# Optimization experiments

Measured on AMD Instinct MI355X. Metric: run time of the kernel, lower is better.

## Reference

```python
import jax, jax.numpy as jnp
import numpy as np

KSIZE = 7
LOSS_WEIGHT = 1.0


def _box_filter(x, ksize):
    # x: (N, 1, H, W) already reflect-padded -> valid conv with ones kernel
    kern = jnp.ones((1, 1, ksize, ksize), x.dtype)
    return jax.lax.conv_general_dilated(
        x, kern, window_strides=(1, 1), padding='VALID',
        dimension_numbers=('NCHW', 'OIHW', 'NCHW'))


def _local_var(residual, ksize):
    # unbiased variance over each ksize x ksize window (reflect padding),
    # computed via box-filtered sum and sum-of-squares (same math as
    # torch.var over unfolded windows, without materializing the windows).
    pad = (ksize - 1) // 2
    rp = jnp.pad(residual, ((0, 0), (0, 0), (pad, pad), (pad, pad)), mode='reflect')
    n = ksize * ksize
    s = _box_filter(rp, ksize)        # window sums
    ss = _box_filter(rp * rp, ksize)  # window sums of squares
    return (ss - s * s / n) / (n - 1)


def setup_inputs() -> dict:
    key = jax.random.key(0)
    k1, k2 = jax.random.split(key)
    shape = (16, 3, 512, 512)
    pred = jax.random.normal(k1, shape, dtype=jnp.float32)
    target = jax.random.normal(k2, shape, dtype=jnp.float32)
    return {"pred": pred, "target": target}


def reference(pred, target):
    # residual over channels: (N, 1, H, W)
    residual = jnp.sum(jnp.abs(target - pred), axis=1, keepdims=True)
    # patch-level weight: unbiased var over (C,H,W), ^(1/5)
    patch_w = jnp.var(residual, axis=(1, 2, 3), keepdims=True, ddof=1) ** 0.2
    # pixel-level weight: local unbiased variance in ksize window
    pixel_w = _local_var(residual, KSIZE)
    overall_weight = patch_w * pixel_w  # (N, 1, H, W), broadcasts over C
    # L1 criterion on weighted pred vs weighted target
    return jnp.mean(jnp.abs(overall_weight * pred - overall_weight * target)) * LOSS_WEIGHT
```

## Files before the change

### kernel.cpp

```cpp
#include <hip/hip_runtime.h>
#include <math.h>

#define N_IMG 16
#define C_CH 3
#define H_DIM 512
#define W_DIM 512
#define HW (H_DIM * W_DIM)
#define KS 7
#define PAD 3

#define TS 32
#define TILE (TS + 2 * PAD)
#define TSTRIDE 40
#define TPB 256
#define TILES_PER_IMG ((H_DIM / TS) * (W_DIM / TS))
#define NBLOCKS (N_IMG * TILES_PER_IMG)


__global__ __launch_bounds__(TPB) void k_fused(const float* __restrict__ pred,
                                               const float* __restrict__ targ,
                                               float* __restrict__ pr,
                                               float* __restrict__ pr2,
                                               float* __restrict__ pc) {
    __shared__ float tile[TILE * TSTRIDE];

    const int bid = blockIdx.x;
    const int n   = bid >> 8;
    const int t   = bid & 255;
    const int by  = t >> 4;
    const int bx  = t & 15;
    const int tid = threadIdx.x;

    const float* p = pred + (size_t)n * C_CH * HW;
    const float* q = targ + (size_t)n * C_CH * HW;

    for (int i = tid; i < TILE * TILE; i += TPB) {
        const int ly = i / TILE;
        const int lx = i - ly * TILE;
        int gy = by * TS - PAD + ly;
        int gx = bx * TS - PAD + lx;
        gy = (gy < 0) ? -gy : ((gy >= H_DIM) ? (2 * H_DIM - 2 - gy) : gy);
        gx = (gx < 0) ? -gx : ((gx >= W_DIM) ? (2 * W_DIM - 2 - gx) : gx);
        const int off = gy * W_DIM + gx;
        const float r = fabsf(q[off] - p[off])
                      + fabsf(q[off + HW] - p[off + HW])
                      + fabsf(q[off + 2 * HW] - p[off + 2 * HW]);
        tile[ly * TSTRIDE + lx] = r;
    }
    __syncthreads();

    const int tx  = tid & 31;
    const int ty0 = (tid >> 5) << 2;

    float colS[KS], colSS[KS];
#pragma unroll
    for (int j = 0; j < KS; ++j) {
        float s = 0.f, ss = 0.f;
#pragma unroll
        for (int dy = 0; dy < KS; ++dy) {
            const float v = tile[(ty0 + dy) * TSTRIDE + tx + j];
            s  += v;
            ss += v * v;
        }
        colS[j] = s; colSS[j] = ss;
    }

    float acc_r = 0.f, acc_r2 = 0.f, acc_c = 0.f;

#pragma unroll
    for (int k = 0; k < 4; ++k) {
        if (k > 0) {
#pragma unroll
            for (int j = 0; j < KS; ++j) {
                const float vn = tile[(ty0 + 6 + k) * TSTRIDE + tx + j];
                const float vo = tile[(ty0 + k - 1) * TSTRIDE + tx + j];
                colS[j]  += vn - vo;
                colSS[j] += vn * vn - vo * vo;
            }
        }
        float S = 0.f, SS = 0.f;
#pragma unroll
        for (int j = 0; j < KS; ++j) { S += colS[j]; SS += colSS[j]; }

        const float pix_var = (SS - S * S * (1.0f / 49.0f)) * (1.0f / 48.0f);
        const float center  = tile[(ty0 + 3 + k) * TSTRIDE + tx + 3];

        acc_r  += center;
        acc_r2 += center * center;
        acc_c  += pix_var * center;
    }

#pragma unroll
    for (int off = 32; off > 0; off >>= 1) {
        acc_r  += __shfl_down(acc_r,  off);
        acc_r2 += __shfl_down(acc_r2, off);
        acc_c  += __shfl_down(acc_c,  off);
    }
    __shared__ float sh_r[4], sh_r2[4], sh_c[4];
    const int lane = tid & 63;
    const int wave = tid >> 6;
    if (lane == 0) { sh_r[wave] = acc_r; sh_r2[wave] = acc_r2; sh_c[wave] = acc_c; }
    __syncthreads();
    if (tid == 0) {
        pr [bid] = sh_r [0] + sh_r [1] + sh_r [2] + sh_r [3];
        pr2[bid] = sh_r2[0] + sh_r2[1] + sh_r2[2] + sh_r2[3];
        pc [bid] = sh_c [0] + sh_c [1] + sh_c [2] + sh_c [3];
    }
}

__global__ void k_final(const float* __restrict__ pr,
                        const float* __restrict__ pr2,
                        const float* __restrict__ pc,
                        float* __restrict__ out) {
    __shared__ double sh[N_IMG];
    const int tid  = threadIdx.x;
    const int w    = tid >> 6;
    const int lane = tid & 63;

    double R = 0.0, R2 = 0.0, Cs = 0.0;
    for (int i = lane; i < TILES_PER_IMG; i += 64) {
        const int idx = w * TILES_PER_IMG + i;
        R  += (double)pr[idx];
        R2 += (double)pr2[idx];
        Cs += (double)pc[idx];
    }
#pragma unroll
    for (int off = 32; off > 0; off >>= 1) {
        R  += __shfl_down(R,  off);
        R2 += __shfl_down(R2, off);
        Cs += __shfl_down(Cs, off);
    }
    if (lane == 0) {
        const double pvar = (R2 - R * R / (double)HW) / (double)(HW - 1);
        sh[w] = pow(pvar, 0.2) * Cs;
    }
    __syncthreads();
    if (tid == 0) {
        double s = 0.0;
        for (int i = 0; i < N_IMG; ++i) s += sh[i];
        out[0] = (float)(s / ((double)N_IMG * C_CH * HW));
    }
}

extern "C" void kernel_launch(void* const* d_in, const int* in_sizes, int n_in,
                              void* d_out, int out_size, void* d_ws, size_t ws_size,
                              hipStream_t stream) {
    const float* pred = (const float*)d_in[0];
    const float* targ = (const float*)d_in[1];

    float* pr  = (float*)d_ws;
    float* pr2 = pr  + NBLOCKS;
    float* pc  = pr2 + NBLOCKS;
    float* out = (float*)d_out;

    k_fused<<<NBLOCKS, TPB, 0, stream>>>(pred, targ, pr, pr2, pc);
    k_final<<<1, 1024, 0, stream>>>(pr, pr2, pc, out);
}
```

Baseline: 144.7 us.

## Enlarge tiles to 64x64 and switch to row-sum sliding window

Tile size grows from 32 to 64, so the reflect halo is a smaller fraction of each tile and fewer global loads are redundant. Each thread now walks 16 rows instead of 4 and keeps a ring buffer of per-row horizontal sums, updating the running window sum and sum of squares with one new row per step. The load loop is unrolled with a fixed trip count, and the final reduction is simplified for 64 tiles per image. Fewer blocks (1024) may lower occupancy and latency hiding, and longer running-sum chains slightly change float rounding.

Measured after the change: 126.8 us. 12.4% less time.

```diff
diff --git a/kernel.cpp b/kernel.cpp
--- a/kernel.cpp
+++ b/kernel.cpp
@@ -9,9 +9,9 @@
 #define KS 7
 #define PAD 3
 
-#define TS 32
+#define TS 64
 #define TILE (TS + 2 * PAD)
-#define TSTRIDE 40
+#define TSTRIDE 72
 #define TPB 256
 #define TILES_PER_IMG ((H_DIM / TS) * (W_DIM / TS))
 #define NBLOCKS (N_IMG * TILES_PER_IMG)
@@ -25,63 +25,85 @@
     __shared__ float tile[TILE * TSTRIDE];
 
     const int bid = blockIdx.x;
-    const int n   = bid >> 8;
-    const int t   = bid & 255;
-    const int by  = t >> 4;
-    const int bx  = t & 15;
+    const int n   = bid >> 6;
+    const int t   = bid & 63;
+    const int by  = t >> 3;
+    const int bx  = t & 7;
     const int tid = threadIdx.x;
 
-    const float* p = pred + (size_t)n * C_CH * HW;
-    const float* q = targ + (size_t)n * C_CH * HW;
+    const float* p0 = pred + (size_t)n * C_CH * HW;
+    const float* p1 = p0 + HW;
+    const float* p2 = p1 + HW;
+    const float* q0 = targ + (size_t)n * C_CH * HW;
+    const float* q1 = q0 + HW;
+    const float* q2 = q1 + HW;
 
-    for (int i = tid; i < TILE * TILE; i += TPB) {
+    const int y0 = by * TS - PAD;
+    const int x0 = bx * TS - PAD;
+#pragma unroll 4
+    for (int it = 0; it < 19; ++it) {
+        const int i  = tid + it * TPB;
         const int ly = i / TILE;
         const int lx = i - ly * TILE;
-        int gy = by * TS - PAD + ly;
-        int gx = bx * TS - PAD + lx;
+        int gy = y0 + ly;
+        int gx = x0 + lx;
         gy = (gy < 0) ? -gy : ((gy >= H_DIM) ? (2 * H_DIM - 2 - gy) : gy);
         gx = (gx < 0) ? -gx : ((gx >= W_DIM) ? (2 * W_DIM - 2 - gx) : gx);
         const int off = gy * W_DIM + gx;
-        const float r = fabsf(q[off] - p[off])
-                      + fabsf(q[off + HW] - p[off + HW])
-                      + fabsf(q[off + 2 * HW] - p[off + 2 * HW]);
-        tile[ly * TSTRIDE + lx] = r;
+        tile[ly * TSTRIDE + lx] = fabsf(q0[off] - p0[off])
+                                + fabsf(q1[off] - p1[off])
+                                + fabsf(q2[off] - p2[off]);
+    }
+    if (tid < 36) {
+        const int i  = tid + 19 * TPB;
+        const int ly = i / TILE;
+        const int lx = i - ly * TILE;
+        int gy = y0 + ly;
+        int gx = x0 + lx;
+        gy = (gy < 0) ? -gy : ((gy >= H_DIM) ? (2 * H_DIM - 2 - gy) : gy);
+        gx = (gx < 0) ? -gx : ((gx >= W_DIM) ? (2 * W_DIM - 2 - gx) : gx);
+        const int off = gy * W_DIM + gx;
+        tile[ly * TSTRIDE + lx] = fabsf(q0[off] - p0[off])
+                                + fabsf(q1[off] - p1[off])
+                                + fabsf(q2[off] - p2[off]);
     }
     __syncthreads();
 
-    const int tx  = tid & 31;
-    const int ty0 = (tid >> 5) << 2;
+    const int tx  = tid & 63;
+    const int ty0 = (tid >> 6) << 4;
 
-    float colS[KS], colSS[KS];
+    float rS[KS], rSS[KS];
+    float S = 0.f, SS = 0.f;
 #pragma unroll
-    for (int j = 0; j < KS; ++j) {
+    for (int dy = 0; dy < KS; ++dy) {
         float s = 0.f, ss = 0.f;
 #pragma unroll
-        for (int dy = 0; dy < KS; ++dy) {
+        for (int j = 0; j < KS; ++j) {
             const float v = tile[(ty0 + dy) * TSTRIDE + tx + j];
             s  += v;
             ss += v * v;
         }
-        colS[j] = s; colSS[j] = ss;
+        rS[dy] = s; rSS[dy] = ss;
+        S += s; SS += ss;
     }
 
     float acc_r = 0.f, acc_r2 = 0.f, acc_c = 0.f;
 
 #pragma unroll
-    for (int k = 0; k < 4; ++k) {
+    for (int k = 0; k < 16; ++k) {
         if (k > 0) {
+            float s = 0.f, ss = 0.f;
 #pragma unroll
             for (int j = 0; j < KS; ++j) {
-                const float vn = tile[(ty0 + 6 + k) * TSTRIDE + tx + j];
-                const float vo = tile[(ty0 + k - 1) * TSTRIDE + tx + j];
-                colS[j]  += vn - vo;
-                colSS[j] += vn * vn - vo * vo;
+                const float v = tile[(ty0 + 6 + k) * TSTRIDE + tx + j];
+                s  += v;
+                ss += v * v;
             }
+            const int slot = (k - 1) % KS;
+            S  += s  - rS[slot];
+            SS += ss - rSS[slot];
+            rS[slot] = s; rSS[slot] = ss;
         }
-        float S = 0.f, SS = 0.f;
-#pragma unroll
-        for (int j = 0; j < KS; ++j) { S += colS[j]; SS += colSS[j]; }
-
         const float pix_var = (SS - S * S * (1.0f / 49.0f)) * (1.0f / 48.0f);
         const float center  = tile[(ty0 + 3 + k) * TSTRIDE + tx + 3];
 
@@ -118,11 +140,11 @@
     const int lane = tid & 63;
 
     double R = 0.0, R2 = 0.0, Cs = 0.0;
-    for (int i = lane; i < TILES_PER_IMG; i += 64) {
-        const int idx = w * TILES_PER_IMG + i;
-        R  += (double)pr[idx];
-        R2 += (double)pr2[idx];
-        Cs += (double)pc[idx];
+    if (lane < TILES_PER_IMG) {
+        const int idx = w * TILES_PER_IMG + lane;
+        R  = (double)pr[idx];
+        R2 = (double)pr2[idx];
+        Cs = (double)pc[idx];
     }
 #pragma unroll
     for (int off = 32; off > 0; off >>= 1) {
```

## Use 64x32 tiles with float4 loads and sliding row-sum box filter

Applied to the files above, without the earlier changes.

Widens each tile to 64x32 pixels, so the reflect-padded halo is a smaller share of each tile. The interior residual is loaded with float4 vector reads of pred and target, and the left and right halo columns are filled by scalar loads. The 7x7 window now slides vertically over cached per-row sums instead of per-column sums, and each thread handles 8 output rows instead of 4. The aim is fewer global memory transactions and less redundant shared-memory and ALU work, at the cost of more registers and half as many blocks.

Result: faster. 127.4 us (-11.9%).

```diff
diff --git a/kernel.cpp b/kernel.cpp
--- a/kernel.cpp
+++ b/kernel.cpp
@@ -9,82 +9,100 @@
 #define KS 7
 #define PAD 3
 
-#define TS 32
-#define TILE (TS + 2 * PAD)
-#define TSTRIDE 40
+#define TSX 64
+#define TSY 32
+#define TILE_H (TSY + 2 * PAD)
+#define TSTRIDE 72
 #define TPB 256
-#define TILES_PER_IMG ((H_DIM / TS) * (W_DIM / TS))
+#define TILES_X (W_DIM / TSX)
+#define TILES_Y (H_DIM / TSY)
+#define TILES_PER_IMG (TILES_X * TILES_Y)
 #define NBLOCKS (N_IMG * TILES_PER_IMG)
 
+__device__ __forceinline__ int reflect_i(int g, int n) {
+    return (g < 0) ? -g : ((g >= n) ? (2 * n - 2 - g) : g);
+}
 
 __global__ __launch_bounds__(TPB) void k_fused(const float* __restrict__ pred,
                                                const float* __restrict__ targ,
                                                float* __restrict__ pr,
                                                float* __restrict__ pr2,
                                                float* __restrict__ pc) {
-    __shared__ float tile[TILE * TSTRIDE];
+    __shared__ __align__(16) float tile[TILE_H * TSTRIDE];
 
     const int bid = blockIdx.x;
-    const int n   = bid >> 8;
-    const int t   = bid & 255;
-    const int by  = t >> 4;
-    const int bx  = t & 15;
+    const int n   = bid >> 7;
+    const int t   = bid & 127;
+    const int by  = t >> 3;
+    const int bx  = t & 7;
     const int tid = threadIdx.x;
 
-    const float* p = pred + (size_t)n * C_CH * HW;
-    const float* q = targ + (size_t)n * C_CH * HW;
+    const int y0 = by * TSY - PAD;
 
-    for (int i = tid; i < TILE * TILE; i += TPB) {
-        const int ly = i / TILE;
-        const int lx = i - ly * TILE;
-        int gy = by * TS - PAD + ly;
-        int gx = bx * TS - PAD + lx;
-        gy = (gy < 0) ? -gy : ((gy >= H_DIM) ? (2 * H_DIM - 2 - gy) : gy);
-        gx = (gx < 0) ? -gx : ((gx >= W_DIM) ? (2 * W_DIM - 2 - gx) : gx);
+    const float*  pb = pred + (size_t)n * C_CH * HW;
+    const float*  qb = targ + (size_t)n * C_CH * HW;
+    const float4* P  = (const float4*)pb;
+    const float4* Q  = (const float4*)qb;
+    const int PL4 = HW / 4;
+
+#pragma unroll
+    for (int it = 0; it < 3; ++it) {
+        const int s = tid + it * TPB;
+        if (it < 2 || tid < 96) {
+            const int row = s >> 4;
+            const int c4  = s & 15;
+            const int gy  = reflect_i(y0 + row, H_DIM);
+            const int off = gy * (W_DIM / 4) + bx * 16 + c4;
+            const float4 p0 = P[off], p1 = P[off + PL4], p2 = P[off + 2 * PL4];
+            const float4 q0 = Q[off], q1 = Q[off + PL4], q2 = Q[off + 2 * PL4];
+            float4 r;
+            r.x = fabsf(q0.x - p0.x) + fabsf(q1.x - p1.x) + fabsf(q2.x - p2.x);
+            r.y = fabsf(q0.y - p0.y) + fabsf(q1.y - p1.y) + fabsf(q2.y - p2.y);
+            r.z = fabsf(q0.z - p0.z) + fabsf(q1.z - p1.z) + fabsf(q2.z - p2.z);
+            r.w = fabsf(q0.w - p0.w) + fabsf(q1.w - p1.w) + fabsf(q2.w - p2.w);
+            *(float4*)&tile[row * TSTRIDE + 4 + c4 * 4] = r;
+        }
+    }
+    if (tid < TILE_H * 6) {
+        const int row = tid / 6;
+        const int k   = tid - row * 6;
+        const int lx  = (k < 3) ? (1 + k) : (65 + k);
+        const int gx  = reflect_i(bx * TSX + lx - 4, W_DIM);
+        const int gy  = reflect_i(y0 + row, H_DIM);
         const int off = gy * W_DIM + gx;
-        const float r = fabsf(q[off] - p[off])
-                      + fabsf(q[off + HW] - p[off + HW])
-                      + fabsf(q[off + 2 * HW] - p[off + 2 * HW]);
-        tile[ly * TSTRIDE + lx] = r;
+        tile[row * TSTRIDE + lx] = fabsf(qb[off] - pb[off])
+                                 + fabsf(qb[off + HW] - pb[off + HW])
+                                 + fabsf(qb[off + 2 * HW] - pb[off + 2 * HW]);
     }
     __syncthreads();
 
-    const int tx  = tid & 31;
-    const int ty0 = (tid >> 5) << 2;
+    const int tx = tid & 63;
+    const int r0 = (tid >> 6) << 3;
 
-    float colS[KS], colSS[KS];
+    float rS[KS], rSS[KS];
+    float S = 0.f, SS = 0.f;
 #pragma unroll
-    for (int j = 0; j < KS; ++j) {
+    for (int d = 0; d < KS; ++d) {
+        const float* rw = &tile[(r0 + d) * TSTRIDE + 1 + tx];
         float s = 0.f, ss = 0.f;
 #pragma unroll
-        for (int dy = 0; dy < KS; ++dy) {
-            const float v = tile[(ty0 + dy) * TSTRIDE + tx + j];
-            s  += v;
-            ss += v * v;
-        }
-        colS[j] = s; colSS[j] = ss;
+        for (int j = 0; j < KS; ++j) { const float v = rw[j]; s += v; ss += v * v; }
+        rS[d] = s; rSS[d] = ss; S += s; SS += ss;
     }
 
     float acc_r = 0.f, acc_r2 = 0.f, acc_c = 0.f;
-
 #pragma unroll
-    for (int k = 0; k < 4; ++k) {
+    for (int k = 0; k < 8; ++k) {
         if (k > 0) {
+            const float* rw = &tile[(r0 + 6 + k) * TSTRIDE + 1 + tx];
+            float s = 0.f, ss = 0.f;
 #pragma unroll
-            for (int j = 0; j < KS; ++j) {
-                const float vn = tile[(ty0 + 6 + k) * TSTRIDE + tx + j];
-                const float vo = tile[(ty0 + k - 1) * TSTRIDE + tx + j];
-                colS[j]  += vn - vo;
-                colSS[j] += vn * vn - vo * vo;
-            }
+            for (int j = 0; j < KS; ++j) { const float v = rw[j]; s += v; ss += v * v; }
+            S  += s  - rS[k - 1];
+            SS += ss - rSS[k - 1];
         }
-        float S = 0.f, SS = 0.f;
-#pragma unroll
-        for (int j = 0; j < KS; ++j) { S += colS[j]; SS += colSS[j]; }
-
         const float pix_var = (SS - S * S * (1.0f / 49.0f)) * (1.0f / 48.0f);
-        const float center  = tile[(ty0 + 3 + k) * TSTRIDE + tx + 3];
-
+        const float center  = tile[(r0 + k + 3) * TSTRIDE + 4 + tx];
         acc_r  += center;
         acc_r2 += center * center;
         acc_c  += pix_var * center;
```
